# Kernel optimization log

Hardware: AMD Instinct MI355X
Metric: run time of the kernel (lower is better)

The kernel has to match this reference:

```python
import jax, jax.numpy as jnp
import numpy as np

N_NODES = 100000
N_EDGES = 640000
D = 128
EPS = 1e-5

def _full_layer_norm(x):
    # torch layer_norm with normalized_shape == x.shape: stats over ALL elements
    mu = jnp.mean(x)
    var = jnp.mean(jnp.square(x - mu))  # biased variance
    return (x - mu) * jax.lax.rsqrt(var + EPS)

def setup_inputs() -> dict:
    key = jax.random.key(0)
    k1, k2, k3, k4, k5 = jax.random.split(key, 5)
    scale1 = 1.0 / np.sqrt(D)
    scale2 = 1.0 / np.sqrt(2 * D)
    return {
        "edge_features": jax.random.normal(k1, (N_EDGES, D), dtype=jnp.float32),
        "node_features": jax.random.normal(k2, (N_NODES, D), dtype=jnp.float32),
        "edge_indices": jax.random.randint(k3, (N_EDGES, 2), 0, N_NODES, dtype=jnp.int32),
        "W1": jax.random.normal(k4, (D, D), dtype=jnp.float32) * scale1,
        "b1": jnp.zeros((D,), dtype=jnp.float32),
        "W2": jax.random.normal(k5, (2 * D, D), dtype=jnp.float32) * scale2,
        "b2": jnp.zeros((D,), dtype=jnp.float32),
    }

def reference(edge_features, node_features, edge_indices, W1, b1, W2, b2):
    # node MLP: linear -> whole-tensor layernorm -> gelu
    h = node_features @ W1 + b1                       # [N, D]
    h = jax.nn.gelu(_full_layer_norm(h), approximate=False)
    # gather source-node features onto edges
    src = edge_indices[:, 0]
    dst = edge_indices[:, 1]
    gathered = h[src]                                 # [E, D]
    e = jnp.concatenate([edge_features, gathered], axis=1)  # [E, 2D]
    e = e @ W2 + b2                                   # [E, D]
    e = jax.nn.gelu(_full_layer_norm(e), approximate=False)
    # scatter-mean (include_self=False): nodes with no in-edges stay 0
    seg_sum = jax.ops.segment_sum(e, dst, num_segments=N_NODES)       # [N, D]
    counts = jax.ops.segment_sum(jnp.ones((e.shape[0],), e.dtype), dst,
                                 num_segments=N_NODES)                 # [N]
    counts = counts[:, None]
    return jnp.where(counts > 0, seg_sum / jnp.maximum(counts, 1.0), 0.0)
```

## Files before the change

### kernel.cpp

```cpp
#include <hip/hip_runtime.h>
#include <hip/hip_bf16.h>
#include <math.h>

typedef __bf16 bf16;
typedef bf16 bf16x8 __attribute__((ext_vector_type(8)));
typedef float f32x4 __attribute__((ext_vector_type(4)));
typedef unsigned short ushort_t;
typedef unsigned long long u64;

#define N_NODES 100000
#define N_EDGES 640000
#define DD 128
#define MAXDEG 64
#define STAT_SCALE 1048576.0

__device__ __forceinline__ float gelu_fast(float x) {
    float z2 = x * (1.595769122f + 0.071354816f * x * x);
    return x * __builtin_amdgcn_rcpf(1.0f + __expf(-z2));
}

__device__ __forceinline__ ushort_t bf16_bits(float x) {
    bf16 h = (bf16)x;
    return __builtin_bit_cast(ushort_t, h);
}

__device__ __forceinline__ float bits_to_f(ushort_t u) {
    return __uint_as_float(((unsigned)u) << 16);
}

__device__ __forceinline__ long long to_fixed(double x) {
    return (long long)(x * STAT_SCALE + (x >= 0.0 ? 0.5 : -0.5));
}

__device__ __forceinline__ void stats_atomic(float lsum, float lsq, float* red,
                                             u64* dsum, u64* dsq) {
    int tid = threadIdx.x;
    red[tid] = lsum; __syncthreads();
    for (int s = 128; s > 0; s >>= 1) { if (tid < s) red[tid] += red[tid + s]; __syncthreads(); }
    float bs = red[0]; __syncthreads();
    red[tid] = lsq; __syncthreads();
    for (int s = 128; s > 0; s >>= 1) { if (tid < s) red[tid] += red[tid + s]; __syncthreads(); }
    if (tid == 0) {
        atomicAdd(dsum, (u64)to_fixed((double)bs));
        atomicAdd(dsq,  (u64)to_fixed((double)red[0]));
    }
}

__device__ __forceinline__ void stats_decode(const u64* stats, double cnt,
                                             float* mu, float* rs) {
    long long ss = (long long)stats[0], sq = (long long)stats[1];
    double mu_d = ((double)ss / STAT_SCALE) / cnt;
    double var  = ((double)sq / STAT_SCALE) / cnt - mu_d * mu_d;
    *mu = (float)mu_d;
    *rs = (float)(1.0 / sqrt(var + 1e-5));
}

#define K1_TILES 1563
__global__ __launch_bounds__(256) void k1_gemm1(
    const float* __restrict__ nf, const float* __restrict__ W1,
    const float* __restrict__ b1, ushort_t* __restrict__ hpre,
    u64* __restrict__ stats, int nblocks)
{
    __shared__ bf16 Ash[64 * 136];
    __shared__ float red[256];
    const int tid = threadIdx.x;
    const int lane = tid & 63;
    const int w = tid >> 6;
    const int l15 = lane & 15, l4 = lane >> 4;

    bf16x8 bfrag[4][2];
    #pragma unroll
    for (int s = 0; s < 4; ++s)
        #pragma unroll
        for (int t = 0; t < 2; ++t) {
            int n = w * 32 + t * 16 + l15;
            #pragma unroll
            for (int j = 0; j < 8; ++j)
                bfrag[s][t][j] = (bf16)W1[(s * 32 + l4 * 8 + j) * DD + n];
        }
    float4 bias4[2];
    bias4[0] = *(const float4*)&b1[w * 32 + l4 * 4];
    bias4[1] = *(const float4*)&b1[w * 32 + 16 + l4 * 4];

    float lsum = 0.f, lsq = 0.f;
    const int srow = tid >> 2;
    const int q = tid & 3;

    for (int tile = blockIdx.x; tile < K1_TILES; tile += nblocks) {
        const int rbase = tile * 64;
        {
            int grow = min(rbase + srow, N_NODES - 1);
            const float4* p = (const float4*)&nf[(size_t)grow * DD + q * 32];
            #pragma unroll
            for (int u = 0; u < 4; ++u) {
                float4 a = p[2 * u], b = p[2 * u + 1];
                ushort_t o[8] = {bf16_bits(a.x), bf16_bits(a.y), bf16_bits(a.z), bf16_bits(a.w),
                                 bf16_bits(b.x), bf16_bits(b.y), bf16_bits(b.z), bf16_bits(b.w)};
                *(uint4*)&Ash[srow * 136 + q * 32 + u * 8] = *(const uint4*)o;
            }
        }
        __syncthreads();
        f32x4 acc[4][2];
        #pragma unroll
        for (int r = 0; r < 4; ++r)
            #pragma unroll
            for (int t = 0; t < 2; ++t)
                acc[r][t] = (f32x4){0.f, 0.f, 0.f, 0.f};
        #pragma unroll
        for (int s = 0; s < 4; ++s)
            #pragma unroll
            for (int r = 0; r < 4; ++r) {
                bf16x8 a = *(const bf16x8*)&Ash[(r * 16 + l15) * 136 + s * 32 + l4 * 8];
                acc[r][0] = __builtin_amdgcn_mfma_f32_16x16x32_bf16(bfrag[s][0], a, acc[r][0], 0, 0, 0);
                acc[r][1] = __builtin_amdgcn_mfma_f32_16x16x32_bf16(bfrag[s][1], a, acc[r][1], 0, 0, 0);
            }
        __syncthreads();
        #pragma unroll
        for (int r = 0; r < 4; ++r) {
            int row = rbase + r * 16 + l15;
            if (row < N_NODES) {
                #pragma unroll
                for (int t = 0; t < 2; ++t) {
                    int col = w * 32 + t * 16 + l4 * 4;
                    ushort_t o[4];
                    #pragma unroll
                    for (int j = 0; j < 4; ++j) {
                        float v = acc[r][t][j] + bias4[t][j];
                        lsum += v; lsq += v * v;
                        o[j] = bf16_bits(v);
                    }
                    *(uint2*)&hpre[(size_t)row * DD + col] = *(const uint2*)o;
                }
            }
        }
    }
    stats_atomic(lsum, lsq, red, &stats[0], &stats[1]);
}

__global__ __launch_bounds__(256) void k3_act(
    const ushort_t* __restrict__ hpre, const u64* __restrict__ stats,
    ushort_t* __restrict__ hg)
{
    float mu, rs;
    stats_decode(stats, (double)N_NODES * DD, &mu, &rs);
    size_t i = (size_t)(blockIdx.x * 256 + threadIdx.x) * 8;
    uint4 v = *(const uint4*)(hpre + i);
    const ushort_t* in = (const ushort_t*)&v;
    ushort_t o[8];
    #pragma unroll
    for (int j = 0; j < 8; ++j)
        o[j] = bf16_bits(gelu_fast((bits_to_f(in[j]) - mu) * rs));
    *(uint4*)(hg + i) = *(const uint4*)o;
}

__global__ __launch_bounds__(256) void k4_gemm2(
    const float* __restrict__ ef, const ushort_t* __restrict__ hg,
    const int* __restrict__ eidx, const float* __restrict__ W2,
    const float* __restrict__ b2, ushort_t* __restrict__ e0,
    u64* __restrict__ stats, int nblocks)
{
    __shared__ bf16 Ash[64 * 264];
    __shared__ float red[256];
    const int tid = threadIdx.x;
    const int lane = tid & 63;
    const int w = tid >> 6;
    const int l15 = lane & 15, l4 = lane >> 4;

    bf16x8 bfrag[8][2];
    #pragma unroll
    for (int s = 0; s < 8; ++s)
        #pragma unroll
        for (int t = 0; t < 2; ++t) {
            int n = w * 32 + t * 16 + l15;
            #pragma unroll
            for (int j = 0; j < 8; ++j)
                bfrag[s][t][j] = (bf16)W2[(s * 32 + l4 * 8 + j) * DD + n];
        }
    float4 bias4[2];
    bias4[0] = *(const float4*)&b2[w * 32 + l4 * 4];
    bias4[1] = *(const float4*)&b2[w * 32 + 16 + l4 * 4];

    float lsum = 0.f, lsq = 0.f;
    const int srow = tid >> 2;
    const int q = tid & 3;

    for (int tile = blockIdx.x; tile < N_EDGES / 64; tile += nblocks) {
        const int ebase = tile * 64;
        {
            const float4* p = (const float4*)&ef[(size_t)(ebase + srow) * DD + q * 32];
            #pragma unroll
            for (int u = 0; u < 4; ++u) {
                float4 a = p[2 * u], b = p[2 * u + 1];
                ushort_t o[8] = {bf16_bits(a.x), bf16_bits(a.y), bf16_bits(a.z), bf16_bits(a.w),
                                 bf16_bits(b.x), bf16_bits(b.y), bf16_bits(b.z), bf16_bits(b.w)};
                *(uint4*)&Ash[srow * 264 + q * 32 + u * 8] = *(const uint4*)o;
            }
            int src = eidx[(size_t)(ebase + srow) * 2];
            const uint4* hp = (const uint4*)&hg[(size_t)src * DD + q * 32];
            uint4* hd = (uint4*)&Ash[srow * 264 + 128 + q * 32];
            #pragma unroll
            for (int u = 0; u < 4; ++u) hd[u] = hp[u];
        }
        __syncthreads();
        f32x4 acc[4][2];
        #pragma unroll
        for (int r = 0; r < 4; ++r)
            #pragma unroll
            for (int t = 0; t < 2; ++t)
                acc[r][t] = (f32x4){0.f, 0.f, 0.f, 0.f};
        #pragma unroll
        for (int s = 0; s < 8; ++s)
            #pragma unroll
            for (int r = 0; r < 4; ++r) {
                bf16x8 a = *(const bf16x8*)&Ash[(r * 16 + l15) * 264 + s * 32 + l4 * 8];
                acc[r][0] = __builtin_amdgcn_mfma_f32_16x16x32_bf16(bfrag[s][0], a, acc[r][0], 0, 0, 0);
                acc[r][1] = __builtin_amdgcn_mfma_f32_16x16x32_bf16(bfrag[s][1], a, acc[r][1], 0, 0, 0);
            }
        __syncthreads();
        #pragma unroll
        for (int r = 0; r < 4; ++r) {
            int row = ebase + r * 16 + l15;
            #pragma unroll
            for (int t = 0; t < 2; ++t) {
                int col = w * 32 + t * 16 + l4 * 4;
                ushort_t o[4];
                #pragma unroll
                for (int j = 0; j < 4; ++j) {
                    float v = acc[r][t][j] + bias4[t][j];
                    lsum += v; lsq += v * v;
                    o[j] = bf16_bits(v);
                }
                *(uint2*)&e0[(size_t)row * DD + col] = *(const uint2*)o;
            }
        }
    }
    stats_atomic(lsum, lsq, red, &stats[2], &stats[3]);
}

__global__ __launch_bounds__(256) void k7_fill(
    const int* __restrict__ eidx, int* __restrict__ cnt, int* __restrict__ slot)
{
    int e = blockIdx.x * 256 + threadIdx.x;
    if (e >= N_EDGES) return;
    int dst = eidx[(size_t)e * 2 + 1];
    int pos = atomicAdd(&cnt[dst], 1);
    if (pos < MAXDEG) slot[dst * MAXDEG + pos] = e;
}

__global__ __launch_bounds__(256) void k8_gather(
    const ushort_t* __restrict__ e0v, const int* __restrict__ slot,
    const int* __restrict__ cnt, const u64* __restrict__ stats,
    float* __restrict__ out)
{
    float mu, rs;
    stats_decode(stats + 2, (double)N_EDGES * DD, &mu, &rs);
    int node = (int)((blockIdx.x * 256 + threadIdx.x) >> 6);
    int lane = threadIdx.x & 63;
    if (node >= N_NODES) return;
    int c = cnt[node];
    int m = min(c, MAXDEG);
    int myslot = (lane < m) ? slot[node * MAXDEG + lane] : 0;
    float a0 = 0.f, a1 = 0.f;
    const size_t off = (size_t)(lane * 2);
    int j = 0;
    for (; j + 4 <= m; j += 4) {
        int ea = __shfl(myslot, j);
        int eb = __shfl(myslot, j + 1);
        int ec = __shfl(myslot, j + 2);
        int ed = __shfl(myslot, j + 3);
        unsigned ua = *(const unsigned*)&e0v[(size_t)ea * DD + off];
        unsigned ub = *(const unsigned*)&e0v[(size_t)eb * DD + off];
        unsigned uc = *(const unsigned*)&e0v[(size_t)ec * DD + off];
        unsigned ud = *(const unsigned*)&e0v[(size_t)ed * DD + off];
        a0 += gelu_fast((__uint_as_float(ua << 16) - mu) * rs);
        a1 += gelu_fast((__uint_as_float(ua & 0xffff0000u) - mu) * rs);
        a0 += gelu_fast((__uint_as_float(ub << 16) - mu) * rs);
        a1 += gelu_fast((__uint_as_float(ub & 0xffff0000u) - mu) * rs);
        a0 += gelu_fast((__uint_as_float(uc << 16) - mu) * rs);
        a1 += gelu_fast((__uint_as_float(uc & 0xffff0000u) - mu) * rs);
        a0 += gelu_fast((__uint_as_float(ud << 16) - mu) * rs);
        a1 += gelu_fast((__uint_as_float(ud & 0xffff0000u) - mu) * rs);
    }
    for (; j < m; ++j) {
        int ea = __shfl(myslot, j);
        unsigned ua = *(const unsigned*)&e0v[(size_t)ea * DD + off];
        a0 += gelu_fast((__uint_as_float(ua << 16) - mu) * rs);
        a1 += gelu_fast((__uint_as_float(ua & 0xffff0000u) - mu) * rs);
    }
    float inv = c > 0 ? 1.0f / (float)c : 0.f;
    float2 res = {a0 * inv, a1 * inv};
    *(float2*)&out[(size_t)node * DD + lane * 2] = res;
}

extern "C" void kernel_launch(void* const* d_in, const int* in_sizes, int n_in,
                              void* d_out, int out_size, void* d_ws, size_t ws_size,
                              hipStream_t stream) {
    const float* ef  = (const float*)d_in[0];
    const float* nf  = (const float*)d_in[1];
    const int*   eix = (const int*)d_in[2];
    const float* W1  = (const float*)d_in[3];
    const float* b1  = (const float*)d_in[4];
    const float* W2  = (const float*)d_in[5];
    const float* b2  = (const float*)d_in[6];
    float* out = (float*)d_out;
    char* ws = (char*)d_ws;

    ushort_t* hpre  = (ushort_t*)(ws + 0);
    ushort_t* hg    = (ushort_t*)(ws + 25600000);
    ushort_t* e0    = (ushort_t*)(ws + 51200000);
    int*      cnt   = (int*)(ws + 215040000);
    u64*      stats = (u64*)(ws + 215440000);
    int*      slot  = (int*)(ws + 215440064);

    hipMemsetAsync(cnt, 0, 400000 + 64, stream);
    k1_gemm1<<<521, 256, 0, stream>>>(nf, W1, b1, hpre, stats, 521);
    k3_act<<<6250, 256, 0, stream>>>(hpre, stats, hg);
    k7_fill<<<2500, 256, 0, stream>>>(eix, cnt, slot);
    k4_gemm2<<<2500, 256, 0, stream>>>(ef, hg, eix, W2, b2, e0, stats, 2500);
    k8_gather<<<25000, 256, 0, stream>>>(e0, slot, cnt, stats, out);
}
```

Baseline: 335.8 us.

## Precompute per-node h@W2 bottom half, gather projected rows in edge GEMM

Splits the edge GEMM algebraically: the gathered-node half of concat@W2 is computed once per node (100k rows) in a new kernel that fuses the layernorm+gelu activation, instead of once per edge (640k rows). The edge GEMM now only multiplies edge_features by the top half of W2 and adds a gathered bf16 row of the precomputed node projection in the epilogue. This halves the MFMA work and LDS footprint in the edge kernel, at the cost of an extra node-level GEMM pass and an extra bf16 rounding of the partial product. Grid sizes for the gemm1 kernel also change.

New measurement: 311.3 us. 7.3% less time.

```diff
diff --git a/kernel.cpp b/kernel.cpp
--- a/kernel.cpp
+++ b/kernel.cpp
@@ -137,38 +137,100 @@
     stats_atomic(lsum, lsq, red, &stats[0], &stats[1]);
 }
 
-__global__ __launch_bounds__(256) void k3_act(
-    const ushort_t* __restrict__ hpre, const u64* __restrict__ stats,
-    ushort_t* __restrict__ hg)
-{
+__global__ __launch_bounds__(256) void k2b_gemmh(
+    const ushort_t* __restrict__ hpre, const float* __restrict__ W2,
+    const u64* __restrict__ stats, ushort_t* __restrict__ hh, int nblocks)
+{
+    __shared__ bf16 Ash[64 * 136];
     float mu, rs;
     stats_decode(stats, (double)N_NODES * DD, &mu, &rs);
-    size_t i = (size_t)(blockIdx.x * 256 + threadIdx.x) * 8;
-    uint4 v = *(const uint4*)(hpre + i);
-    const ushort_t* in = (const ushort_t*)&v;
-    ushort_t o[8];
+
+    const int tid = threadIdx.x;
+    const int lane = tid & 63;
+    const int w = tid >> 6;
+    const int l15 = lane & 15, l4 = lane >> 4;
+
+    bf16x8 bfrag[4][2];
     #pragma unroll
-    for (int j = 0; j < 8; ++j)
-        o[j] = bf16_bits(gelu_fast((bits_to_f(in[j]) - mu) * rs));
-    *(uint4*)(hg + i) = *(const uint4*)o;
+    for (int s = 0; s < 4; ++s)
+        #pragma unroll
+        for (int t = 0; t < 2; ++t) {
+            int n = w * 32 + t * 16 + l15;
+            #pragma unroll
+            for (int j = 0; j < 8; ++j)
+                bfrag[s][t][j] = (bf16)W2[(DD + s * 32 + l4 * 8 + j) * DD + n];
+        }
+
+    const int srow = tid >> 2;
+    const int q = tid & 3;
+
+    for (int tile = blockIdx.x; tile < K1_TILES; tile += nblocks) {
+        const int rbase = tile * 64;
+        {
+            int grow = min(rbase + srow, N_NODES - 1);
+            const uint4* p = (const uint4*)&hpre[(size_t)grow * DD + q * 32];
+            #pragma unroll
+            for (int u = 0; u < 4; ++u) {
+                uint4 v = p[u];
+                const ushort_t* in = (const ushort_t*)&v;
+                ushort_t o[8];
+                #pragma unroll
+                for (int j = 0; j < 8; ++j)
+                    o[j] = bf16_bits(gelu_fast((bits_to_f(in[j]) - mu) * rs));
+                *(uint4*)&Ash[srow * 136 + q * 32 + u * 8] = *(const uint4*)o;
+            }
+        }
+        __syncthreads();
+        f32x4 acc[4][2];
+        #pragma unroll
+        for (int r = 0; r < 4; ++r)
+            #pragma unroll
+            for (int t = 0; t < 2; ++t)
+                acc[r][t] = (f32x4){0.f, 0.f, 0.f, 0.f};
+        #pragma unroll
+        for (int s = 0; s < 4; ++s)
+            #pragma unroll
+            for (int r = 0; r < 4; ++r) {
+                bf16x8 a = *(const bf16x8*)&Ash[(r * 16 + l15) * 136 + s * 32 + l4 * 8];
+                acc[r][0] = __builtin_amdgcn_mfma_f32_16x16x32_bf16(bfrag[s][0], a, acc[r][0], 0, 0, 0);
+                acc[r][1] = __builtin_amdgcn_mfma_f32_16x16x32_bf16(bfrag[s][1], a, acc[r][1], 0, 0, 0);
+            }
+        __syncthreads();
+        #pragma unroll
+        for (int r = 0; r < 4; ++r) {
+            int row = rbase + r * 16 + l15;
+            if (row < N_NODES) {
+                #pragma unroll
+                for (int t = 0; t < 2; ++t) {
+                    int col = w * 32 + t * 16 + l4 * 4;
+                    ushort_t o[4];
+                    #pragma unroll
+                    for (int j = 0; j < 4; ++j)
+                        o[j] = bf16_bits(acc[r][t][j]);
+                    *(uint2*)&hh[(size_t)row * DD + col] = *(const uint2*)o;
+                }
+            }
+        }
+    }
 }
 
 __global__ __launch_bounds__(256) void k4_gemm2(
-    const float* __restrict__ ef, const ushort_t* __restrict__ hg,
+    const float* __restrict__ ef, const ushort_t* __restrict__ hh,
     const int* __restrict__ eidx, const float* __restrict__ W2,
     const float* __restrict__ b2, ushort_t* __restrict__ e0,
     u64* __restrict__ stats, int nblocks)
 {
-    __shared__ bf16 Ash[64 * 264];
+    __shared__ bf16 Ash[64 * 136];
+    __shared__ int Ssrc[64];
     __shared__ float red[256];
     const int tid = threadIdx.x;
     const int lane = tid & 63;
     const int w = tid >> 6;
     const int l15 = lane & 15, l4 = lane >> 4;
 
-    bf16x8 bfrag[8][2];
+    bf16x8 bfrag[4][2];
     #pragma unroll
-    for (int s = 0; s < 8; ++s)
+    for (int s = 0; s < 4; ++s)
         #pragma unroll
         for (int t = 0; t < 2; ++t) {
             int n = w * 32 + t * 16 + l15;
@@ -193,13 +255,9 @@
                 float4 a = p[2 * u], b = p[2 * u + 1];
                 ushort_t o[8] = {bf16_bits(a.x), bf16_bits(a.y), bf16_bits(a.z), bf16_bits(a.w),
                                  bf16_bits(b.x), bf16_bits(b.y), bf16_bits(b.z), bf16_bits(b.w)};
-                *(uint4*)&Ash[srow * 264 + q * 32 + u * 8] = *(const uint4*)o;
-            }
-            int src = eidx[(size_t)(ebase + srow) * 2];
-            const uint4* hp = (const uint4*)&hg[(size_t)src * DD + q * 32];
-            uint4* hd = (uint4*)&Ash[srow * 264 + 128 + q * 32];
-            #pragma unroll
-            for (int u = 0; u < 4; ++u) hd[u] = hp[u];
+                *(uint4*)&Ash[srow * 136 + q * 32 + u * 8] = *(const uint4*)o;
+            }
+            if (tid < 64) Ssrc[tid] = eidx[(size_t)(ebase + tid) * 2];
         }
         __syncthreads();
         f32x4 acc[4][2];
@@ -209,13 +267,16 @@
             for (int t = 0; t < 2; ++t)
                 acc[r][t] = (f32x4){0.f, 0.f, 0.f, 0.f};
         #pragma unroll
-        for (int s = 0; s < 8; ++s)
+        for (int s = 0; s < 4; ++s)
             #pragma unroll
             for (int r = 0; r < 4; ++r) {
-                bf16x8 a = *(const bf16x8*)&Ash[(r * 16 + l15) * 264 + s * 32 + l4 * 8];
+                bf16x8 a = *(const bf16x8*)&Ash[(r * 16 + l15) * 136 + s * 32 + l4 * 8];
                 acc[r][0] = __builtin_amdgcn_mfma_f32_16x16x32_bf16(bfrag[s][0], a, acc[r][0], 0, 0, 0);
                 acc[r][1] = __builtin_amdgcn_mfma_f32_16x16x32_bf16(bfrag[s][1], a, acc[r][1], 0, 0, 0);
             }
+        int srows[4];
+        #pragma unroll
+        for (int r = 0; r < 4; ++r) srows[r] = Ssrc[r * 16 + l15];
         __syncthreads();
         #pragma unroll
         for (int r = 0; r < 4; ++r) {
@@ -223,10 +284,16 @@
             #pragma unroll
             for (int t = 0; t < 2; ++t) {
                 int col = w * 32 + t * 16 + l4 * 4;
+                uint2 hv = *(const uint2*)&hh[(size_t)srows[r] * DD + col];
+                float h0 = bits_to_f((ushort_t)(hv.x & 0xffff));
+                float h1 = bits_to_f((ushort_t)(hv.x >> 16));
+                float h2 = bits_to_f((ushort_t)(hv.y & 0xffff));
+                float h3 = bits_to_f((ushort_t)(hv.y >> 16));
+                float hadd[4] = {h0, h1, h2, h3};
                 ushort_t o[4];
                 #pragma unroll
                 for (int j = 0; j < 4; ++j) {
-                    float v = acc[r][t][j] + bias4[t][j];
+                    float v = acc[r][t][j] + bias4[t][j] + hadd[j];
                     lsum += v; lsq += v * v;
                     o[j] = bf16_bits(v);
                 }
@@ -306,16 +373,16 @@
     char* ws = (char*)d_ws;
 
     ushort_t* hpre  = (ushort_t*)(ws + 0);
-    ushort_t* hg    = (ushort_t*)(ws + 25600000);
+    ushort_t* hh    = (ushort_t*)(ws + 25600000);
     ushort_t* e0    = (ushort_t*)(ws + 51200000);
     int*      cnt   = (int*)(ws + 215040000);
     u64*      stats = (u64*)(ws + 215440000);
     int*      slot  = (int*)(ws + 215440064);
 
-    hipMemsetAsync(cnt, 0, 400000 + 64, stream);
-    k1_gemm1<<<521, 256, 0, stream>>>(nf, W1, b1, hpre, stats, 521);
-    k3_act<<<6250, 256, 0, stream>>>(hpre, stats, hg);
+    hipMemsetAsync(cnt, 0, 400064, stream);
+    k1_gemm1<<<782, 256, 0, stream>>>(nf, W1, b1, hpre, stats, 782);
+    k2b_gemmh<<<782, 256, 0, stream>>>(hpre, W2, stats, hh, 782);
     k7_fill<<<2500, 256, 0, stream>>>(eix, cnt, slot);
-    k4_gemm2<<<2500, 256, 0, stream>>>(ef, hg, eix, W2, b2, e0, stats, 2500);
+    k4_gemm2<<<2500, 256, 0, stream>>>(ef, hh, eix, W2, b2, e0, stats, 2500);
     k8_gather<<<25000, 256, 0, stream>>>(e0, slot, cnt, stats, out);
 }
```
